# Kernel optimization log

Measured on AMD Instinct MI355X. Metric: run time of the kernel, lower is better.

Reference implementation:

```python
import jax, jax.numpy as jnp
import numpy as np

B, S, R, H = 256, 196, 1024, 512  # batch, att regions, rnn_size, att_hid_size


def setup_inputs() -> dict:
    key = jax.random.key(0)
    ks = jax.random.split(key, 8)
    return {
        "att_feats": jax.random.normal(ks[0], (B, S, R), dtype=jnp.float32),
        "p_att_feats": jax.random.normal(ks[1], (B, S, H), dtype=jnp.float32),
        "hidden": jax.random.normal(ks[2], (B, R), dtype=jnp.float32),
        "in_weights": jax.random.uniform(ks[3], (B, S), dtype=jnp.float32),
        "h2att_w": jax.random.normal(ks[4], (H, R), dtype=jnp.float32) * (1.0 / np.sqrt(R)),
        "h2att_b": jnp.full((H,), 0.1, dtype=jnp.float32),
        "alpha_w": jax.random.normal(ks[5], (1, H), dtype=jnp.float32) * (1.0 / np.sqrt(H)),
        "alpha_b": jnp.full((1,), 0.1, dtype=jnp.float32),
    }


def reference(att_feats, p_att_feats, hidden, in_weights, h2att_w, h2att_b, alpha_w, alpha_b):
    # att = in_weights * p_att_feats          [B, S, H]
    att = in_weights[:, :, None] * p_att_feats
    # att_h = h2att(hidden)                   [B, H] broadcast over S
    att_h = hidden @ h2att_w.T + h2att_b
    dot = jnp.tanh(att + att_h[:, None, :])   # [B, S, H]
    # alpha_net: Linear(H, 1) -> scores       [B, S]
    scores = jnp.einsum('bsh,h->bs', dot, alpha_w[0]) + alpha_b[0]
    weight = jax.nn.softmax(scores, axis=-1)  # [B, S]
    # weighted pooling: bmm(weight[:,None,:], att_feats).squeeze(1)
    att_res = jnp.einsum('bs,bsr->br', weight, att_feats)  # [B, R]
    return (att_res, weight)
```

## Files before the change

### kernel.cpp

```cpp
#include <hip/hip_runtime.h>
#include <math.h>

#define BN 256
#define SN 196
#define RN 1024
#define HN 512
#define KSPLIT 8
#define KCH 128
#define PSPLIT 8

__device__ __forceinline__ float fast_tanh(float x) {
    float e = __expf(2.0f * x);
    return 1.0f - 2.0f * __builtin_amdgcn_rcpf(e + 1.0f);
}

__global__ __launch_bounds__(256) void k_gemm_partial(
    const float* __restrict__ hidden, const float* __restrict__ w,
    float* __restrict__ partial) {
    __shared__ float At[64][64];
    __shared__ float Bt[64][64];
    const int t  = threadIdx.x;
    const int b0 = blockIdx.x * 64;
    const int h0 = blockIdx.y * 64;
    const int kc = blockIdx.z;

    const int th4 = (t & 15) * 4;
    const int tb4 = (t >> 4) * 4;
    float4 acc0 = {0,0,0,0}, acc1 = {0,0,0,0}, acc2 = {0,0,0,0}, acc3 = {0,0,0,0};

    for (int sub = 0; sub < 2; ++sub) {
        const int k0 = kc * KCH + sub * 64;
        {
            const int row = t >> 2, kq = (t & 3) * 16;
            const float* srcA = hidden + (size_t)(b0 + row) * RN + k0 + kq;
            const float* srcB = w      + (size_t)(h0 + row) * RN + k0 + kq;
#pragma unroll
            for (int j = 0; j < 4; ++j) {
                float4 v = *(const float4*)(srcA + j * 4);
                int k = kq + j * 4;
                At[k][row] = v.x; At[k+1][row] = v.y; At[k+2][row] = v.z; At[k+3][row] = v.w;
            }
#pragma unroll
            for (int j = 0; j < 4; ++j) {
                float4 v = *(const float4*)(srcB + j * 4);
                int k = kq + j * 4;
                Bt[k][row] = v.x; Bt[k+1][row] = v.y; Bt[k+2][row] = v.z; Bt[k+3][row] = v.w;
            }
        }
        __syncthreads();
#pragma unroll 8
        for (int k = 0; k < 64; ++k) {
            float4 a  = *(const float4*)&At[k][tb4];
            float4 bb = *(const float4*)&Bt[k][th4];
            acc0.x = fmaf(a.x, bb.x, acc0.x); acc0.y = fmaf(a.x, bb.y, acc0.y);
            acc0.z = fmaf(a.x, bb.z, acc0.z); acc0.w = fmaf(a.x, bb.w, acc0.w);
            acc1.x = fmaf(a.y, bb.x, acc1.x); acc1.y = fmaf(a.y, bb.y, acc1.y);
            acc1.z = fmaf(a.y, bb.z, acc1.z); acc1.w = fmaf(a.y, bb.w, acc1.w);
            acc2.x = fmaf(a.z, bb.x, acc2.x); acc2.y = fmaf(a.z, bb.y, acc2.y);
            acc2.z = fmaf(a.z, bb.z, acc2.z); acc2.w = fmaf(a.z, bb.w, acc2.w);
            acc3.x = fmaf(a.w, bb.x, acc3.x); acc3.y = fmaf(a.w, bb.y, acc3.y);
            acc3.z = fmaf(a.w, bb.z, acc3.z); acc3.w = fmaf(a.w, bb.w, acc3.w);
        }
        __syncthreads();
    }
    float* dst = partial + ((size_t)kc * BN + b0 + tb4) * HN + h0 + th4;
    *(float4*)(dst)          = acc0;
    *(float4*)(dst + HN)     = acc1;
    *(float4*)(dst + 2 * HN) = acc2;
    *(float4*)(dst + 3 * HN) = acc3;
}

__global__ __launch_bounds__(1024) void k_scores(
    const float* __restrict__ partial, const float* __restrict__ bias,
    const float* __restrict__ p_att, const float* __restrict__ in_w,
    const float* __restrict__ alpha_w, float* __restrict__ weight_out) {
    __shared__ float att_h[HN];
    __shared__ float sc[256];
    const int b    = blockIdx.x;
    const int t    = threadIdx.x;
    const int wv   = t >> 6;
    const int lane = t & 63;

    if (t >= SN && t < 256) sc[t] = -1e30f;

    if (t < 128) {
        float4 s = *(const float4*)(bias + t * 4);
        const float* p = partial + (size_t)b * HN + t * 4;
#pragma unroll
        for (int kc = 0; kc < KSPLIT; ++kc) {
            float4 v = *(const float4*)(p + (size_t)kc * BN * HN);
            s.x += v.x; s.y += v.y; s.z += v.z; s.w += v.w;
        }
        *(float4*)&att_h[t * 4] = s;
    }
    __syncthreads();

    {
        const float4* a4 = (const float4*)alpha_w;
        const float4 aw0 = a4[lane], aw1 = a4[lane + 64];
        const float4 ah0 = *(const float4*)&att_h[lane * 4];
        const float4 ah1 = *(const float4*)&att_h[(lane + 64) * 4];
        const float4* p4 = (const float4*)p_att;
        for (int si = wv; si < SN; si += 32) {
            const int  sj = si + 16;
            const bool h2 = (sj < SN);
            const float iw0 = in_w[b * SN + si];
            const float iw1 = h2 ? in_w[b * SN + sj] : 0.0f;
            const size_t r0 = (size_t)(b * SN + si) * (HN / 4);
            const size_t r1 = (size_t)(b * SN + (h2 ? sj : si)) * (HN / 4);
            float4 x00 = p4[r0 + lane], x01 = p4[r0 + lane + 64];
            float4 x10 = p4[r1 + lane], x11 = p4[r1 + lane + 64];
            float s0, s1;
            s0  = fast_tanh(fmaf(iw0, x00.x, ah0.x)) * aw0.x;
            s1  = fast_tanh(fmaf(iw1, x10.x, ah0.x)) * aw0.x;
            s0 += fast_tanh(fmaf(iw0, x00.y, ah0.y)) * aw0.y;
            s1 += fast_tanh(fmaf(iw1, x10.y, ah0.y)) * aw0.y;
            s0 += fast_tanh(fmaf(iw0, x00.z, ah0.z)) * aw0.z;
            s1 += fast_tanh(fmaf(iw1, x10.z, ah0.z)) * aw0.z;
            s0 += fast_tanh(fmaf(iw0, x00.w, ah0.w)) * aw0.w;
            s1 += fast_tanh(fmaf(iw1, x10.w, ah0.w)) * aw0.w;
            s0 += fast_tanh(fmaf(iw0, x01.x, ah1.x)) * aw1.x;
            s1 += fast_tanh(fmaf(iw1, x11.x, ah1.x)) * aw1.x;
            s0 += fast_tanh(fmaf(iw0, x01.y, ah1.y)) * aw1.y;
            s1 += fast_tanh(fmaf(iw1, x11.y, ah1.y)) * aw1.y;
            s0 += fast_tanh(fmaf(iw0, x01.z, ah1.z)) * aw1.z;
            s1 += fast_tanh(fmaf(iw1, x11.z, ah1.z)) * aw1.z;
            s0 += fast_tanh(fmaf(iw0, x01.w, ah1.w)) * aw1.w;
            s1 += fast_tanh(fmaf(iw1, x11.w, ah1.w)) * aw1.w;
#pragma unroll
            for (int off = 32; off; off >>= 1) {
                s0 += __shfl_xor(s0, off, 64);
                s1 += __shfl_xor(s1, off, 64);
            }
            if (lane == 0) {
                sc[si] = s0;
                if (h2) sc[sj] = s1;
            }
        }
    }
    __syncthreads();

    if (wv == 0) {
        float v0 = sc[lane], v1 = sc[lane + 64], v2 = sc[lane + 128], v3 = sc[lane + 192];
        float m = fmaxf(fmaxf(v0, v1), fmaxf(v2, v3));
#pragma unroll
        for (int off = 32; off; off >>= 1) m = fmaxf(m, __shfl_xor(m, off, 64));
        float e0 = __expf(v0 - m), e1 = __expf(v1 - m);
        float e2 = __expf(v2 - m), e3 = __expf(v3 - m);
        float s = e0 + e1 + e2 + e3;
#pragma unroll
        for (int off = 32; off; off >>= 1) s += __shfl_xor(s, off, 64);
        float inv = 1.0f / s;
        e0 *= inv; e1 *= inv; e2 *= inv; e3 *= inv;
        float* wo = weight_out + (size_t)b * SN;
        wo[lane] = e0; wo[lane + 64] = e1; wo[lane + 128] = e2;
        if (lane + 192 < SN) wo[lane + 192] = e3;
    }
}

__global__ __launch_bounds__(256) void k_pool(
    const float* __restrict__ weight, const float* __restrict__ att_feats,
    float* __restrict__ pool_part) {
    __shared__ float wsm[32];
    const int b  = blockIdx.x, sq = blockIdx.y;
    const int t  = threadIdx.x, q = t >> 6, lane = t & 63;
    const int base = sq * 24 + (sq < 4 ? sq : 4);
    const int cnt  = 24 + (sq < 4 ? 1 : 0);
    if (t < cnt) wsm[t] = weight[b * SN + base + t];
    __syncthreads();

    const float* src = att_feats + (size_t)b * SN * RN + (size_t)base * RN
                     + q * 256 + lane * 4;
    float4 acc = {0, 0, 0, 0};
    int i = 0;
    for (; i + 5 <= cnt; i += 5) {
#pragma unroll
        for (int j = 0; j < 5; ++j) {
            float ws = wsm[i + j];
            float4 v = *(const float4*)(src + (size_t)(i + j) * RN);
            acc.x = fmaf(ws, v.x, acc.x);
            acc.y = fmaf(ws, v.y, acc.y);
            acc.z = fmaf(ws, v.z, acc.z);
            acc.w = fmaf(ws, v.w, acc.w);
        }
    }
#pragma unroll
    for (; i < cnt; ++i) {
        float ws = wsm[i];
        float4 v = *(const float4*)(src + (size_t)i * RN);
        acc.x = fmaf(ws, v.x, acc.x);
        acc.y = fmaf(ws, v.y, acc.y);
        acc.z = fmaf(ws, v.z, acc.z);
        acc.w = fmaf(ws, v.w, acc.w);
    }
    float* dst = pool_part + ((size_t)sq * BN + b) * RN + q * 256 + lane * 4;
    *(float4*)dst = acc;
}

__global__ __launch_bounds__(256) void k_reduce(
    const float* __restrict__ pool_part, float* __restrict__ att_res) {
    const int e = blockIdx.x * 256 + threadIdx.x;
    float s = 0.0f;
#pragma unroll
    for (int sq = 0; sq < PSPLIT; ++sq)
        s += pool_part[(size_t)sq * BN * RN + e];
    att_res[e] = s;
}

extern "C" void kernel_launch(void* const* d_in, const int* in_sizes, int n_in,
                              void* d_out, int out_size, void* d_ws, size_t ws_size,
                              hipStream_t stream) {
    const float* att_feats   = (const float*)d_in[0];
    const float* p_att_feats = (const float*)d_in[1];
    const float* hidden      = (const float*)d_in[2];
    const float* in_weights  = (const float*)d_in[3];
    const float* h2att_w     = (const float*)d_in[4];
    const float* h2att_b     = (const float*)d_in[5];
    const float* alpha_w     = (const float*)d_in[6];

    float* att_res = (float*)d_out;
    float* weight  = (float*)d_out + BN * RN;
    float* partial   = (float*)d_ws;
    float* pool_part = (float*)d_ws + (size_t)KSPLIT * BN * HN;

    k_gemm_partial<<<dim3(BN / 64, HN / 64, KSPLIT), 256, 0, stream>>>(
        hidden, h2att_w, partial);
    k_scores<<<BN, 1024, 0, stream>>>(partial, h2att_b, p_att_feats, in_weights,
                                      alpha_w, weight);
    k_pool<<<dim3(BN, PSPLIT), 256, 0, stream>>>(weight, att_feats, pool_part);
    k_reduce<<<(BN * RN) / 256, 256, 0, stream>>>(pool_part, att_res);
}
```

Before: 371.5 us.

## Split score kernel across S chunks and move softmax into pool kernel

```diff
diff --git a/kernel.cpp b/kernel.cpp
--- a/kernel.cpp
+++ b/kernel.cpp
@@ -7,6 +7,7 @@
 #define HN 512
 #define KSPLIT 8
 #define KCH 128
+#define SSPLIT 8
 #define PSPLIT 8
 
 __device__ __forceinline__ float fast_tanh(float x) {
@@ -70,18 +71,19 @@
     *(float4*)(dst + 3 * HN) = acc3;
 }
 
-__global__ __launch_bounds__(1024) void k_scores(
+__global__ __launch_bounds__(256) void k_scores(
     const float* __restrict__ partial, const float* __restrict__ bias,
     const float* __restrict__ p_att, const float* __restrict__ in_w,
-    const float* __restrict__ alpha_w, float* __restrict__ weight_out) {
+    const float* __restrict__ alpha_w, float* __restrict__ sc_out) {
     __shared__ float att_h[HN];
-    __shared__ float sc[256];
+    __shared__ float wsm[32];
     const int b    = blockIdx.x;
+    const int sq   = blockIdx.y;
     const int t    = threadIdx.x;
     const int wv   = t >> 6;
     const int lane = t & 63;
-
-    if (t >= SN && t < 256) sc[t] = -1e30f;
+    const int base = sq * 24 + (sq < 4 ? sq : 4);
+    const int cnt  = 24 + (sq < 4 ? 1 : 0);
 
     if (t < 128) {
         float4 s = *(const float4*)(bias + t * 4);
@@ -93,82 +95,81 @@
         }
         *(float4*)&att_h[t * 4] = s;
     }
-    __syncthreads();
-
-    {
-        const float4* a4 = (const float4*)alpha_w;
-        const float4 aw0 = a4[lane], aw1 = a4[lane + 64];
-        const float4 ah0 = *(const float4*)&att_h[lane * 4];
-        const float4 ah1 = *(const float4*)&att_h[(lane + 64) * 4];
-        const float4* p4 = (const float4*)p_att;
-        for (int si = wv; si < SN; si += 32) {
-            const int  sj = si + 16;
-            const bool h2 = (sj < SN);
-            const float iw0 = in_w[b * SN + si];
-            const float iw1 = h2 ? in_w[b * SN + sj] : 0.0f;
-            const size_t r0 = (size_t)(b * SN + si) * (HN / 4);
-            const size_t r1 = (size_t)(b * SN + (h2 ? sj : si)) * (HN / 4);
-            float4 x00 = p4[r0 + lane], x01 = p4[r0 + lane + 64];
-            float4 x10 = p4[r1 + lane], x11 = p4[r1 + lane + 64];
-            float s0, s1;
-            s0  = fast_tanh(fmaf(iw0, x00.x, ah0.x)) * aw0.x;
-            s1  = fast_tanh(fmaf(iw1, x10.x, ah0.x)) * aw0.x;
-            s0 += fast_tanh(fmaf(iw0, x00.y, ah0.y)) * aw0.y;
-            s1 += fast_tanh(fmaf(iw1, x10.y, ah0.y)) * aw0.y;
-            s0 += fast_tanh(fmaf(iw0, x00.z, ah0.z)) * aw0.z;
-            s1 += fast_tanh(fmaf(iw1, x10.z, ah0.z)) * aw0.z;
-            s0 += fast_tanh(fmaf(iw0, x00.w, ah0.w)) * aw0.w;
-            s1 += fast_tanh(fmaf(iw1, x10.w, ah0.w)) * aw0.w;
-            s0 += fast_tanh(fmaf(iw0, x01.x, ah1.x)) * aw1.x;
-            s1 += fast_tanh(fmaf(iw1, x11.x, ah1.x)) * aw1.x;
-            s0 += fast_tanh(fmaf(iw0, x01.y, ah1.y)) * aw1.y;
-            s1 += fast_tanh(fmaf(iw1, x11.y, ah1.y)) * aw1.y;
-            s0 += fast_tanh(fmaf(iw0, x01.z, ah1.z)) * aw1.z;
-            s1 += fast_tanh(fmaf(iw1, x11.z, ah1.z)) * aw1.z;
-            s0 += fast_tanh(fmaf(iw0, x01.w, ah1.w)) * aw1.w;
-            s1 += fast_tanh(fmaf(iw1, x11.w, ah1.w)) * aw1.w;
-#pragma unroll
-            for (int off = 32; off; off >>= 1) {
-                s0 += __shfl_xor(s0, off, 64);
-                s1 += __shfl_xor(s1, off, 64);
-            }
-            if (lane == 0) {
-                sc[si] = s0;
-                if (h2) sc[sj] = s1;
-            }
-        }
-    }
-    __syncthreads();
-
-    if (wv == 0) {
-        float v0 = sc[lane], v1 = sc[lane + 64], v2 = sc[lane + 128], v3 = sc[lane + 192];
-        float m = fmaxf(fmaxf(v0, v1), fmaxf(v2, v3));
-#pragma unroll
-        for (int off = 32; off; off >>= 1) m = fmaxf(m, __shfl_xor(m, off, 64));
-        float e0 = __expf(v0 - m), e1 = __expf(v1 - m);
-        float e2 = __expf(v2 - m), e3 = __expf(v3 - m);
-        float s = e0 + e1 + e2 + e3;
-#pragma unroll
-        for (int off = 32; off; off >>= 1) s += __shfl_xor(s, off, 64);
-        float inv = 1.0f / s;
-        e0 *= inv; e1 *= inv; e2 *= inv; e3 *= inv;
-        float* wo = weight_out + (size_t)b * SN;
-        wo[lane] = e0; wo[lane + 64] = e1; wo[lane + 128] = e2;
-        if (lane + 192 < SN) wo[lane + 192] = e3;
+    if (t < cnt) wsm[t] = in_w[b * SN + base + t];
+    __syncthreads();
+
+    const float4* a4 = (const float4*)alpha_w;
+    const float4 aw0 = a4[lane], aw1 = a4[lane + 64];
+    const float4 ah0 = *(const float4*)&att_h[lane * 4];
+    const float4 ah1 = *(const float4*)&att_h[(lane + 64) * 4];
+    const float4* p4 = (const float4*)p_att;
+    for (int i = wv; i < cnt; i += 8) {
+        const int  j  = i + 4;
+        const bool h2 = (j < cnt);
+        const float iw0 = wsm[i];
+        const float iw1 = h2 ? wsm[j] : 0.0f;
+        const size_t r0 = (size_t)(b * SN + base + i) * (HN / 4);
+        const size_t r1 = (size_t)(b * SN + base + (h2 ? j : i)) * (HN / 4);
+        float4 x00 = p4[r0 + lane], x01 = p4[r0 + lane + 64];
+        float4 x10 = p4[r1 + lane], x11 = p4[r1 + lane + 64];
+        float s0, s1;
+        s0  = fast_tanh(fmaf(iw0, x00.x, ah0.x)) * aw0.x;
+        s1  = fast_tanh(fmaf(iw1, x10.x, ah0.x)) * aw0.x;
+        s0 += fast_tanh(fmaf(iw0, x00.y, ah0.y)) * aw0.y;
+        s1 += fast_tanh(fmaf(iw1, x10.y, ah0.y)) * aw0.y;
+        s0 += fast_tanh(fmaf(iw0, x00.z, ah0.z)) * aw0.z;
+        s1 += fast_tanh(fmaf(iw1, x10.z, ah0.z)) * aw0.z;
+        s0 += fast_tanh(fmaf(iw0, x00.w, ah0.w)) * aw0.w;
+        s1 += fast_tanh(fmaf(iw1, x10.w, ah0.w)) * aw0.w;
+        s0 += fast_tanh(fmaf(iw0, x01.x, ah1.x)) * aw1.x;
+        s1 += fast_tanh(fmaf(iw1, x11.x, ah1.x)) * aw1.x;
+        s0 += fast_tanh(fmaf(iw0, x01.y, ah1.y)) * aw1.y;
+        s1 += fast_tanh(fmaf(iw1, x11.y, ah1.y)) * aw1.y;
+        s0 += fast_tanh(fmaf(iw0, x01.z, ah1.z)) * aw1.z;
+        s1 += fast_tanh(fmaf(iw1, x11.z, ah1.z)) * aw1.z;
+        s0 += fast_tanh(fmaf(iw0, x01.w, ah1.w)) * aw1.w;
+        s1 += fast_tanh(fmaf(iw1, x11.w, ah1.w)) * aw1.w;
+#pragma unroll
+        for (int off = 32; off; off >>= 1) {
+            s0 += __shfl_xor(s0, off, 64);
+            s1 += __shfl_xor(s1, off, 64);
+        }
+        if (lane == 0) {
+            sc_out[b * SN + base + i] = s0;
+            if (h2) sc_out[b * SN + base + j] = s1;
+        }
     }
 }
 
 __global__ __launch_bounds__(256) void k_pool(
-    const float* __restrict__ weight, const float* __restrict__ att_feats,
-    float* __restrict__ pool_part) {
-    __shared__ float wsm[32];
+    const float* __restrict__ sc_in, const float* __restrict__ att_feats,
+    float* __restrict__ pool_part, float* __restrict__ weight_out) {
+    __shared__ float sc[256];
+    __shared__ float wred[8];
     const int b  = blockIdx.x, sq = blockIdx.y;
     const int t  = threadIdx.x, q = t >> 6, lane = t & 63;
+
+    float v = (t < SN) ? sc_in[b * SN + t] : -1e30f;
+    float m = v;
+#pragma unroll
+    for (int off = 32; off; off >>= 1) m = fmaxf(m, __shfl_xor(m, off, 64));
+    if (lane == 0) wred[q] = m;
+    __syncthreads();
+    m = fmaxf(fmaxf(wred[0], wred[1]), fmaxf(wred[2], wred[3]));
+    float e = (t < SN) ? __expf(v - m) : 0.0f;
+    float s = e;
+#pragma unroll
+    for (int off = 32; off; off >>= 1) s += __shfl_xor(s, off, 64);
+    if (lane == 0) wred[4 + q] = s;
+    __syncthreads();
+    s = (wred[4] + wred[5]) + (wred[6] + wred[7]);
+    const float wnorm = e * (1.0f / s);
+    sc[t] = wnorm;
+    if (sq == 0 && t < SN) weight_out[b * SN + t] = wnorm;
+    __syncthreads();
+
     const int base = sq * 24 + (sq < 4 ? sq : 4);
     const int cnt  = 24 + (sq < 4 ? 1 : 0);
-    if (t < cnt) wsm[t] = weight[b * SN + base + t];
-    __syncthreads();
-
     const float* src = att_feats + (size_t)b * SN * RN + (size_t)base * RN
                      + q * 256 + lane * 4;
     float4 acc = {0, 0, 0, 0};
@@ -176,22 +177,22 @@
     for (; i + 5 <= cnt; i += 5) {
 #pragma unroll
         for (int j = 0; j < 5; ++j) {
-            float ws = wsm[i + j];
-            float4 v = *(const float4*)(src + (size_t)(i + j) * RN);
-            acc.x = fmaf(ws, v.x, acc.x);
-            acc.y = fmaf(ws, v.y, acc.y);
-            acc.z = fmaf(ws, v.z, acc.z);
-            acc.w = fmaf(ws, v.w, acc.w);
+            float ws = sc[base + i + j];
+            float4 vv = *(const float4*)(src + (size_t)(i + j) * RN);
+            acc.x = fmaf(ws, vv.x, acc.x);
+            acc.y = fmaf(ws, vv.y, acc.y);
+            acc.z = fmaf(ws, vv.z, acc.z);
+            acc.w = fmaf(ws, vv.w, acc.w);
         }
     }
 #pragma unroll
     for (; i < cnt; ++i) {
-        float ws = wsm[i];
-        float4 v = *(const float4*)(src + (size_t)i * RN);
-        acc.x = fmaf(ws, v.x, acc.x);
-        acc.y = fmaf(ws, v.y, acc.y);
-        acc.z = fmaf(ws, v.z, acc.z);
-        acc.w = fmaf(ws, v.w, acc.w);
+        float ws = sc[base + i];
+        float4 vv = *(const float4*)(src + (size_t)i * RN);
+        acc.x = fmaf(ws, vv.x, acc.x);
+        acc.y = fmaf(ws, vv.y, acc.y);
+        acc.z = fmaf(ws, vv.z, acc.z);
+        acc.w = fmaf(ws, vv.w, acc.w);
     }
     float* dst = pool_part + ((size_t)sq * BN + b) * RN + q * 256 + lane * 4;
     *(float4*)dst = acc;
@@ -221,12 +222,14 @@
     float* att_res = (float*)d_out;
     float* weight  = (float*)d_out + BN * RN;
     float* partial   = (float*)d_ws;
-    float* pool_part = (float*)d_ws + (size_t)KSPLIT * BN * HN;
+    float* pool_part = partial + (size_t)KSPLIT * BN * HN;
+    float* sc_raw    = pool_part + (size_t)PSPLIT * BN * RN;
 
     k_gemm_partial<<<dim3(BN / 64, HN / 64, KSPLIT), 256, 0, stream>>>(
         hidden, h2att_w, partial);
-    k_scores<<<BN, 1024, 0, stream>>>(partial, h2att_b, p_att_feats, in_weights,
-                                      alpha_w, weight);
-    k_pool<<<dim3(BN, PSPLIT), 256, 0, stream>>>(weight, att_feats, pool_part);
+    k_scores<<<dim3(BN, SSPLIT), 256, 0, stream>>>(
+        partial, h2att_b, p_att_feats, in_weights, alpha_w, sc_raw);
+    k_pool<<<dim3(BN, PSPLIT), 256, 0, stream>>>(
+        sc_raw, att_feats, pool_part, weight);
     k_reduce<<<(BN * RN) / 256, 256, 0, stream>>>(pool_part, att_res);
 }
```

After: 371.9 us. Within noise of the previous version (+0.1%).
